# Kernel optimization log

Measured on AMD Instinct MI355X. Metric: run time of the kernel, lower is better.

## Reference

```python
import jax, jax.numpy as jnp
import numpy as np

IN_F = 4096
OUT_F = 4096
WBITS = 4      # weight bits
ABITS = 4      # input (activation) bits; T=4 -> L=ceil(15/4)=4 spike levels/step
EPS = 1e-8


def fwht(x):
    """Normalized fast Walsh-Hadamard transform over the last dim (K=1 case of
    matmul_hadU_cuda): y = H_n @ x / sqrt(n), n a power of 2."""
    n = x.shape[-1]
    m = int(np.log2(n))
    shape = x.shape
    x = x.reshape((-1,) + (2,) * m)  # [B, 2,2,...,2]
    for ax in range(1, m + 1):       # fixed log2(n) butterfly stages
        a = jnp.take(x, 0, axis=ax)
        b = jnp.take(x, 1, axis=ax)
        x = jnp.stack([a + b, a - b], axis=ax)
    return x.reshape(shape) * np.float32(1.0 / np.sqrt(n))


def quant_weight(w):
    """Per-output-channel symmetric RTN fake-quant to WBITS, with STE."""
    qmax = 2 ** (WBITS - 1) - 1  # 7
    scale = jnp.maximum(jnp.max(jnp.abs(w), axis=1, keepdims=True) / qmax, EPS)
    q = jnp.clip(jnp.round(w / scale), -qmax - 1, qmax)
    wq = q * scale
    return w + jax.lax.stop_gradient(wq - w)


def quant_act(x):
    """LMHT spiking input quantizer: dynamic asymmetric fake-quant to ABITS.
    Over T steps the neuron emits up to L levels/step, summing to the integer
    code q in [0, 2^ABITS-1]; the (averaged) dequantized output equals
    (q - zp) * scale. STE for gradient."""
    levels = 2 ** ABITS - 1  # 15
    xmin = jnp.min(x)
    xmax = jnp.max(x)
    scale = jnp.maximum((xmax - xmin) / levels, EPS)
    zp = jnp.round(-xmin / scale)
    q = jnp.clip(jnp.round(x / scale) + zp, 0, levels)
    xq = (q - zp) * scale
    return x + jax.lax.stop_gradient(xq - x)


def setup_inputs() -> dict:
    key = jax.random.key(0)
    k1, k2, k3 = jax.random.split(key, 3)
    x = jax.random.normal(k1, (4, 2048, IN_F), dtype=jnp.float32)
    weight = jax.random.normal(k2, (OUT_F, IN_F), dtype=jnp.float32) * 0.02
    bias = jax.random.normal(k3, (OUT_F,), dtype=jnp.float32) * 0.01
    return {"x": x, "weight": weight, "bias": bias}


def reference(x, weight, bias):
    # online full Hadamard rotation of the input
    x = fwht(x)
    # weight fake-quant (W4) and activation fake-quant (A4, LMHT neuron)
    wq = quant_weight(weight)
    xq = quant_act(x)
    # F.linear: out = xq @ wq.T + bias
    out = jnp.einsum('bsi,oi->bso', xq, wq) + bias
    return out
```

## Files before the change

kernel.cpp:

```cpp
#include <hip/hip_runtime.h>
#include <stdint.h>
#include <stddef.h>


typedef __attribute__((ext_vector_type(4))) int int4v;
typedef __attribute__((ext_vector_type(4))) float float4v;

#define EPSQ 1e-8f

__device__ __forceinline__ void fwht_wave(float (&e)[64], int l) {
#pragma unroll
    for (int s = 32; s >= 4; s >>= 1)
#pragma unroll
        for (int j = 0; j < 64; ++j)
            if ((j & s) == 0) {
                float a = e[j], b = e[j + s];
                e[j] = a + b;
                e[j + s] = a - b;
            }
#pragma unroll
    for (int m = 32; m >= 1; m >>= 1) {
        float sgn = (l & m) ? -1.0f : 1.0f;
#pragma unroll
        for (int j = 0; j < 64; ++j) {
            float t = __shfl_xor(e[j], m);
            e[j] = fmaf(sgn, e[j], t);
        }
    }
#pragma unroll
    for (int s = 2; s >= 1; s >>= 1)
#pragma unroll
        for (int j = 0; j < 64; ++j)
            if ((j & s) == 0) {
                float a = e[j], b = e[j + s];
                e[j] = a + b;
                e[j + s] = a - b;
            }
}

__device__ __forceinline__ void load_row(const float* __restrict__ xr, int l,
                                         float (&e)[64]) {
    const float4v* xv = (const float4v*)xr;
#pragma unroll
    for (int q = 0; q < 16; ++q) {
        float4v v = xv[q * 64 + l];
        e[4 * q + 0] = v[0]; e[4 * q + 1] = v[1];
        e[4 * q + 2] = v[2]; e[4 * q + 3] = v[3];
    }
}

__global__ __launch_bounds__(256) void k_fwht_minmax(
    const float* __restrict__ x, float2* __restrict__ wmm) {
    int l = threadIdx.x & 63, w = threadIdx.x >> 6;
    int row = blockIdx.x * 4 + w;
    float e[64];
    load_row(x + (size_t)row * 4096, l, e);
    fwht_wave(e, l);
    float mn = e[0], mx = e[0];
#pragma unroll
    for (int j = 1; j < 64; ++j) { mn = fminf(mn, e[j]); mx = fmaxf(mx, e[j]); }
#pragma unroll
    for (int m = 32; m >= 1; m >>= 1) {
        mn = fminf(mn, __shfl_xor(mn, m));
        mx = fmaxf(mx, __shfl_xor(mx, m));
    }
    if (l == 0) wmm[row] = make_float2(mn * 0.015625f, mx * 0.015625f);
}

__global__ __launch_bounds__(256) void k_mmred(const float2* __restrict__ wmm,
                                               float* __restrict__ mm) {
    __shared__ float red[8];
    int t = threadIdx.x;
    float mn = INFINITY, mx = -INFINITY;
    for (int i = t; i < 8192; i += 256) {
        float2 v = wmm[i];
        mn = fminf(mn, v.x);
        mx = fmaxf(mx, v.y);
    }
#pragma unroll
    for (int m = 32; m >= 1; m >>= 1) {
        mn = fminf(mn, __shfl_xor(mn, m));
        mx = fmaxf(mx, __shfl_xor(mx, m));
    }
    if ((t & 63) == 0) { red[(t >> 6) * 2] = mn; red[(t >> 6) * 2 + 1] = mx; }
    __syncthreads();
    if (t == 0) {
#pragma unroll
        for (int wv = 1; wv < 4; ++wv) {
            mn = fminf(mn, red[wv * 2]);
            mx = fmaxf(mx, red[wv * 2 + 1]);
        }
        mm[0] = mn;
        mm[1] = mx;
    }
}

__global__ __launch_bounds__(256) void k_quant_x(
    const float* __restrict__ x, const float* __restrict__ mm,
    int8_t* __restrict__ xq) {
    int l = threadIdx.x & 63, w = threadIdx.x >> 6;
    int row = blockIdx.x * 4 + w;
    float e[64];
    load_row(x + (size_t)row * 4096, l, e);
    fwht_wave(e, l);

    float xmin = mm[0], xmax = mm[1];
    float scale = fmaxf((xmax - xmin) / 15.0f, EPSQ);
    float zp = rintf(-xmin / scale);
    int izp = (int)zp;

    int* qrow = (int*)(xq + (size_t)row * 4096);
#pragma unroll
    for (int q = 0; q < 16; ++q) {
        int pk = 0;
#pragma unroll
        for (int r = 0; r < 4; ++r) {
            float v = e[4 * q + r] * 0.015625f;
            float qq = rintf(v / scale) + zp;
            qq = fminf(fmaxf(qq, 0.0f), 15.0f);
            int code = (int)qq - izp;
            pk |= (code & 0xFF) << (8 * r);
        }
        qrow[q * 64 + l] = pk;
    }
}

__global__ __launch_bounds__(256) void k_quant_w(
    const float* __restrict__ wgt, int8_t* __restrict__ wq,
    float* __restrict__ sw) {
    __shared__ float red[4];
    int o = blockIdx.x, t = threadIdx.x;
    const float4v* wv = (const float4v*)(wgt + (size_t)o * 4096);
    float4v a0 = wv[t * 4 + 0], a1 = wv[t * 4 + 1],
            a2 = wv[t * 4 + 2], a3 = wv[t * 4 + 3];
    float am = 0.0f;
#pragma unroll
    for (int r = 0; r < 4; ++r)
        am = fmaxf(am, fmaxf(fmaxf(fabsf(a0[r]), fabsf(a1[r])),
                             fmaxf(fabsf(a2[r]), fabsf(a3[r]))));
#pragma unroll
    for (int m = 32; m >= 1; m >>= 1) am = fmaxf(am, __shfl_xor(am, m));
    if ((t & 63) == 0) red[t >> 6] = am;
    __syncthreads();
    am = fmaxf(fmaxf(red[0], red[1]), fmaxf(red[2], red[3]));

    float scale = fmaxf(am / 7.0f, EPSQ);
    if (t == 0) sw[o] = scale;

    int4v pk;
#pragma unroll
    for (int k = 0; k < 4; ++k) {
        float4v a = (k == 0) ? a0 : (k == 1) ? a1 : (k == 2) ? a2 : a3;
        int p = 0;
#pragma unroll
        for (int r = 0; r < 4; ++r) {
            float q = rintf(a[r] / scale);
            q = fminf(fmaxf(q, -8.0f), 7.0f);
            p |= ((int)q & 0xFF) << (8 * r);
        }
        pk[k] = p;
    }
    *(int4v*)(wq + (size_t)o * 4096 + t * 16) = pk;
}

#define BM 128
#define BN 128
#define BKq 64

__global__ __launch_bounds__(256) void k_gemm(
    const int8_t* __restrict__ A,
    const int8_t* __restrict__ B,
    const float* __restrict__ sw, const float* __restrict__ bias,
    const float* __restrict__ mm, float* __restrict__ C) {
    constexpr int N = 4096, K = 4096;
    __shared__ __align__(16) int8_t As[BM * BKq];
    __shared__ __align__(16) int8_t Bs[BN * BKq];

    int tid = threadIdx.x;
    int m0 = (blockIdx.x >> 5) * BM;
    int n0 = (blockIdx.x & 31) * BN;
    int w = tid >> 6, l = tid & 63;
    int wr = w >> 1, wc = w & 1;
    int kg = l >> 4, lr = l & 15;

    int4v acc[4][4] = {};

    for (int k0 = 0; k0 < K; k0 += BKq) {
#pragma unroll
        for (int it = 0; it < 2; ++it) {
            int idx = it * 256 + tid;
            int row = idx >> 2, cc = idx & 3;
            __builtin_amdgcn_global_load_lds(
                (const __attribute__((address_space(1))) void*)
                    (A + (size_t)(m0 + row) * K + k0 + cc * 16),
                (__attribute__((address_space(3))) void*)(As + idx * 16),
                16, 0, 0);
            __builtin_amdgcn_global_load_lds(
                (const __attribute__((address_space(1))) void*)
                    (B + (size_t)(n0 + row) * K + k0 + cc * 16),
                (__attribute__((address_space(3))) void*)(Bs + idx * 16),
                16, 0, 0);
        }
        __syncthreads();

        int4v af[4], bf[4];
#pragma unroll
        for (int i = 0; i < 4; ++i) {
            af[i] = *(const int4v*)(As + (wr * 64 + i * 16 + lr) * BKq + kg * 16);
            bf[i] = *(const int4v*)(Bs + (wc * 64 + i * 16 + lr) * BKq + kg * 16);
        }
#pragma unroll
        for (int i = 0; i < 4; ++i)
#pragma unroll
            for (int j = 0; j < 4; ++j)
                acc[i][j] = __builtin_amdgcn_mfma_i32_16x16x64_i8(
                    af[i], bf[j], acc[i][j], 0, 0, 0);
        __syncthreads();
    }

    float xmin = mm[0], xmax = mm[1];
    float sx = fmaxf((xmax - xmin) / 15.0f, EPSQ);

#pragma unroll
    for (int j = 0; j < 4; ++j) {
        int col = n0 + wc * 64 + j * 16 + lr;
        float s = sx * sw[col];
        float bz = bias[col];
#pragma unroll
        for (int i = 0; i < 4; ++i) {
            int rowb = m0 + wr * 64 + i * 16 + kg * 4;
#pragma unroll
            for (int r = 0; r < 4; ++r)
                C[(size_t)(rowb + r) * N + col] =
                    (float)acc[i][j][r] * s + bz;
        }
    }
}

extern "C" void kernel_launch(void* const* d_in, const int* in_sizes, int n_in,
                              void* d_out, int out_size, void* d_ws,
                              size_t ws_size, hipStream_t stream) {
    const float* x = (const float*)d_in[0];
    const float* weight = (const float*)d_in[1];
    const float* bias = (const float*)d_in[2];
    float* out = (float*)d_out;

    char* ws = (char*)d_ws;
    float* mm = (float*)ws;
    float2* wmm = (float2*)(ws + 1024);
    float* sw = (float*)(ws + 131072);
    int8_t* xq = (int8_t*)(ws + (1 << 20));
    int8_t* wq = (int8_t*)(ws + (1 << 20) + ((size_t)8192 * 4096));

    hipLaunchKernelGGL(k_fwht_minmax, dim3(2048), dim3(256), 0, stream, x, wmm);
    hipLaunchKernelGGL(k_mmred, dim3(1), dim3(256), 0, stream, wmm, mm);
    hipLaunchKernelGGL(k_quant_w, dim3(4096), dim3(256), 0, stream, weight, wq, sw);
    hipLaunchKernelGGL(k_quant_x, dim3(2048), dim3(256), 0, stream, x, mm, xq);
    hipLaunchKernelGGL(k_gemm, dim3(64 * 32), dim3(256), 0, stream,
                       xq, wq, sw, bias, mm, out);
}
```

Measured before the change: 479.7 us.

## Store rotated activations once and XOR-swizzle GEMM LDS tiles

The first pass now writes the Hadamard-rotated, normalized activations into the output buffer, which serves as scratch, so the quantize pass becomes a simple grid-stride elementwise kernel and the FWHT is no longer run twice. This trades recomputation for an extra 128MB write plus a read of the fp32 intermediate. Separately, the GEMM's LDS tile layout is XOR-swizzled on 16-byte chunks by row, to cut bank conflicts on the fragment reads.

Measured after the change: 465.9 us. 1.03x faster.

```diff
diff --git a/kernel.cpp b/kernel.cpp
--- a/kernel.cpp
+++ b/kernel.cpp
@@ -38,24 +38,31 @@
             }
 }
 
-__device__ __forceinline__ void load_row(const float* __restrict__ xr, int l,
-                                         float (&e)[64]) {
-    const float4v* xv = (const float4v*)xr;
+__global__ __launch_bounds__(256) void k_fwht_store(
+    const float* __restrict__ x, float* __restrict__ y,
+    float2* __restrict__ wmm) {
+    int l = threadIdx.x & 63, w = threadIdx.x >> 6;
+    int row = blockIdx.x * 4 + w;
+    const float4v* xv = (const float4v*)(x + (size_t)row * 4096);
+    float e[64];
 #pragma unroll
     for (int q = 0; q < 16; ++q) {
         float4v v = xv[q * 64 + l];
         e[4 * q + 0] = v[0]; e[4 * q + 1] = v[1];
         e[4 * q + 2] = v[2]; e[4 * q + 3] = v[3];
     }
-}
-
-__global__ __launch_bounds__(256) void k_fwht_minmax(
-    const float* __restrict__ x, float2* __restrict__ wmm) {
-    int l = threadIdx.x & 63, w = threadIdx.x >> 6;
-    int row = blockIdx.x * 4 + w;
-    float e[64];
-    load_row(x + (size_t)row * 4096, l, e);
     fwht_wave(e, l);
+#pragma unroll
+    for (int j = 0; j < 64; ++j) e[j] *= 0.015625f;
+
+    float4v* yv = (float4v*)(y + (size_t)row * 4096);
+#pragma unroll
+    for (int q = 0; q < 16; ++q) {
+        float4v v;
+        v[0] = e[4 * q + 0]; v[1] = e[4 * q + 1];
+        v[2] = e[4 * q + 2]; v[3] = e[4 * q + 3];
+        yv[q * 64 + l] = v;
+    }
     float mn = e[0], mx = e[0];
 #pragma unroll
     for (int j = 1; j < 64; ++j) { mn = fminf(mn, e[j]); mx = fmaxf(mx, e[j]); }
@@ -64,7 +71,7 @@
         mn = fminf(mn, __shfl_xor(mn, m));
         mx = fmaxf(mx, __shfl_xor(mx, m));
     }
-    if (l == 0) wmm[row] = make_float2(mn * 0.015625f, mx * 0.015625f);
+    if (l == 0) wmm[row] = make_float2(mn, mx);
 }
 
 __global__ __launch_bounds__(256) void k_mmred(const float2* __restrict__ wmm,
@@ -96,32 +103,29 @@
 }
 
 __global__ __launch_bounds__(256) void k_quant_x(
-    const float* __restrict__ x, const float* __restrict__ mm,
+    const float* __restrict__ y, const float* __restrict__ mm,
     int8_t* __restrict__ xq) {
-    int l = threadIdx.x & 63, w = threadIdx.x >> 6;
-    int row = blockIdx.x * 4 + w;
-    float e[64];
-    load_row(x + (size_t)row * 4096, l, e);
-    fwht_wave(e, l);
-
     float xmin = mm[0], xmax = mm[1];
     float scale = fmaxf((xmax - xmin) / 15.0f, EPSQ);
     float zp = rintf(-xmin / scale);
     int izp = (int)zp;
 
-    int* qrow = (int*)(xq + (size_t)row * 4096);
-#pragma unroll
-    for (int q = 0; q < 16; ++q) {
+    const float4v* yv = (const float4v*)y;
+    int* q = (int*)xq;
+    const size_t n4 = (size_t)8192 * 4096 / 4;
+    const size_t stride = (size_t)2048 * 256;
+    for (size_t i = (size_t)blockIdx.x * 256 + threadIdx.x; i < n4;
+         i += stride) {
+        float4v v = yv[i];
         int pk = 0;
 #pragma unroll
         for (int r = 0; r < 4; ++r) {
-            float v = e[4 * q + r] * 0.015625f;
-            float qq = rintf(v / scale) + zp;
+            float qq = rintf(v[r] / scale) + zp;
             qq = fminf(fmaxf(qq, 0.0f), 15.0f);
             int code = (int)qq - izp;
             pk |= (code & 0xFF) << (8 * r);
         }
-        qrow[q * 64 + l] = pk;
+        q[i] = pk;
     }
 }
 
@@ -189,15 +193,16 @@
 #pragma unroll
         for (int it = 0; it < 2; ++it) {
             int idx = it * 256 + tid;
-            int row = idx >> 2, cc = idx & 3;
+            int row = idx >> 2;
+            int ccs = (idx & 3) ^ ((row >> 1) & 3);
             __builtin_amdgcn_global_load_lds(
                 (const __attribute__((address_space(1))) void*)
-                    (A + (size_t)(m0 + row) * K + k0 + cc * 16),
+                    (A + (size_t)(m0 + row) * K + k0 + ccs * 16),
                 (__attribute__((address_space(3))) void*)(As + idx * 16),
                 16, 0, 0);
             __builtin_amdgcn_global_load_lds(
                 (const __attribute__((address_space(1))) void*)
-                    (B + (size_t)(n0 + row) * K + k0 + cc * 16),
+                    (B + (size_t)(n0 + row) * K + k0 + ccs * 16),
                 (__attribute__((address_space(3))) void*)(Bs + idx * 16),
                 16, 0, 0);
         }
@@ -206,8 +211,12 @@
         int4v af[4], bf[4];
 #pragma unroll
         for (int i = 0; i < 4; ++i) {
-            af[i] = *(const int4v*)(As + (wr * 64 + i * 16 + lr) * BKq + kg * 16);
-            bf[i] = *(const int4v*)(Bs + (wc * 64 + i * 16 + lr) * BKq + kg * 16);
+            int ra = wr * 64 + i * 16 + lr;
+            int rb = wc * 64 + i * 16 + lr;
+            af[i] = *(const int4v*)(As + ra * BKq +
+                                    ((kg ^ ((ra >> 1) & 3)) * 16));
+            bf[i] = *(const int4v*)(Bs + rb * BKq +
+                                    ((kg ^ ((rb >> 1) & 3)) * 16));
         }
 #pragma unroll
         for (int i = 0; i < 4; ++i)
@@ -252,10 +261,15 @@
     int8_t* xq = (int8_t*)(ws + (1 << 20));
     int8_t* wq = (int8_t*)(ws + (1 << 20) + ((size_t)8192 * 4096));
 
-    hipLaunchKernelGGL(k_fwht_minmax, dim3(2048), dim3(256), 0, stream, x, wmm);
+    float* y = out;
+
+    hipLaunchKernelGGL(k_fwht_store, dim3(2048), dim3(256), 0, stream,
+                       x, y, wmm);
     hipLaunchKernelGGL(k_mmred, dim3(1), dim3(256), 0, stream, wmm, mm);
-    hipLaunchKernelGGL(k_quant_w, dim3(4096), dim3(256), 0, stream, weight, wq, sw);
-    hipLaunchKernelGGL(k_quant_x, dim3(2048), dim3(256), 0, stream, x, mm, xq);
+    hipLaunchKernelGGL(k_quant_w, dim3(4096), dim3(256), 0, stream,
+                       weight, wq, sw);
+    hipLaunchKernelGGL(k_quant_x, dim3(2048), dim3(256), 0, stream,
+                       y, mm, xq);
     hipLaunchKernelGGL(k_gemm, dim3(64 * 32), dim3(256), 0, stream,
                        xq, wq, sw, bias, mm, out);
 }
```
